# Kernel tuning notes

Hardware: AMD Instinct MI355X
Metric: run time of the kernel (lower is better)

## Reference

```python
import jax, jax.numpy as jnp
import numpy as np

EPS = 1e-5  # torch BatchNorm2d default eps
K = 3       # kernel_size
D = 1       # dilation (== padding)


def setup_inputs() -> dict:
    key = jax.random.key(0)
    k0, k1, k2 = jax.random.split(key, 3)
    N, C, H, W, O = 4, 2048, 32, 32, 256
    return {
        "x": jax.random.normal(k0, (N, C, H, W), jnp.float32),
        "conv_w": jax.random.normal(k1, (K * K, C, K, K), jnp.float32) * 0.01,
        "gamma": jnp.ones((K * K,), jnp.float32),
        "beta": jnp.zeros((K * K,), jnp.float32),
        "weight": jax.random.normal(k2, (O, C, K * K), jnp.float32) * 0.01,
    }


def reference(x, conv_w, gamma, beta, weight):
    n, c, h, w = x.shape
    # --- dynamic-kernel generator: conv (stride 1, pad=dilation) -> BN (train mode) -> softmax over K*K ---
    sigma = jax.lax.conv_general_dilated(
        x, conv_w, window_strides=(1, 1), padding=[(D, D), (D, D)],
        rhs_dilation=(D, D), dimension_numbers=("NCHW", "OIHW", "NCHW"))  # (n, K*K, h, w)
    mean = sigma.mean(axis=(0, 2, 3), keepdims=True)
    var = sigma.var(axis=(0, 2, 3), keepdims=True)  # biased variance, as torch BN uses for normalization
    sigma = (sigma - mean) * jax.lax.rsqrt(var + EPS)
    sigma = sigma * gamma[None, :, None, None] + beta[None, :, None, None]
    sigma = jax.nn.softmax(sigma, axis=1)            # softmax over the K*K kernel positions
    sigma = sigma.reshape(n, K * K, h * w)           # (n, K*K, h*w)
    # --- unfold (im2col), channel-major (C, kh, kw) ordering matching torch F.unfold ---
    patches = jax.lax.conv_general_dilated_patches(
        x, (K, K), (1, 1), [(D, D), (D, D)], rhs_dilation=(D, D),
        dimension_numbers=("NCHW", "OIHW", "NCHW"))  # (n, C*K*K, h, w)
    patches = patches.reshape(n, c, K * K, h * w)     # (n, C, K*K, h*w)
    # --- per-pixel dynamic weighting + learned projection ---
    # out[n,o,m] = sum_{c,l} patches[n,c,l,m] * sigma[n,l,m] * weight[o,c,l]
    out = jnp.einsum("nclm,nlm,ocl->nom", patches, sigma, weight)
    return out.reshape(n, weight.shape[0], h, w)
```

## Files before the change

kernel.cpp:

```cpp
#include <hip/hip_runtime.h>
#include <hip/hip_bf16.h>
#include <stdint.h>

typedef unsigned short u16;
typedef __attribute__((ext_vector_type(8))) short short8;
typedef __attribute__((ext_vector_type(4))) float floatx4;

#define N_IMG 4
#define C_IN  2048
#define HW    1024
#define KK    9
#define O_OUT 256
#define NPIX  4096
#define M_PAD  2432
#define K_DIM  2048
#define BN_EPS 1e-5f

#define OFF_A    0u
#define OFF_XT   9961472u
#define OFF_H    26738688u
#define OFF_SRAW 46661632u
#define OFF_STAT 46809088u

__device__ __forceinline__ u16 f2b(float f) {
    unsigned u = __float_as_uint(f);
    return (u16)((u + 0x7FFFu + ((u >> 16) & 1u)) >> 16);
}

__device__ __forceinline__ void load8f(const float* base, size_t eidx, u16* out) {
    const float* p = base + eidx;
    float4 a = ((const float4*)p)[0];
    float4 b = ((const float4*)p)[1];
    float f[8] = {a.x, a.y, a.z, a.w, b.x, b.y, b.z, b.w};
#pragma unroll
    for (int j = 0; j < 8; ++j) out[j] = f2b(f[j]);
}

__global__ void build_all(const float* __restrict__ x, const float* __restrict__ wgt,
                          const float* __restrict__ cw, u16* __restrict__ xt,
                          u16* __restrict__ A, float* __restrict__ stats) {
    __shared__ __align__(16) u16 lds[9 * 2056];
    int b = blockIdx.x, t = threadIdx.x;
    if (b < 2048) {
        int c0 = (b & 31) * 64, p0 = ((b >> 5) & 15) * 64, n = b >> 9;
        int r = t >> 3, pv = (t & 7) * 8;
        u16 h0[8], h1[8];
        load8f(x, (size_t)(n * C_IN + c0 + r) * HW + p0 + pv, h0);
        load8f(x, (size_t)(n * C_IN + c0 + r + 32) * HW + p0 + pv, h1);
#pragma unroll
        for (int j = 0; j < 8; ++j) {
            lds[(pv + j) * 72 + r]      = h0[j];
            lds[(pv + j) * 72 + r + 32] = h1[j];
        }
        __syncthreads();
        int pr = t >> 3, cv = (t & 7) * 8;
        uint4 o0 = *(const uint4*)&lds[pr * 72 + cv];
        uint4 o1 = *(const uint4*)&lds[(pr + 32) * 72 + cv];
        *(uint4*)(xt + (size_t)(n * HW + p0 + pr) * K_DIM + c0 + cv) = o0;
        *(uint4*)(xt + (size_t)(n * HW + p0 + pr + 32) * K_DIM + c0 + cv) = o1;
    } else if (b < 2304) {
        int o = b - 2048;
        size_t base = (size_t)o * 18432;
        for (int i = 0; i < 9; ++i) {
            int e0 = (t + i * 256) * 8;
            u16 hv[8];
            load8f(wgt, base + e0, hv);
#pragma unroll
            for (int j = 0; j < 8; ++j) {
                int e = e0 + j;
                int c = e / 9, l = e - c * 9;
                lds[l * 2056 + c] = hv[j];
            }
        }
        __syncthreads();
        for (int l = 0; l < 9; ++l) {
            size_t row = (size_t)l * 256 + o;
            *(uint4*)(A + row * K_DIM + t * 8) = *(const uint4*)&lds[l * 2056 + t * 8];
        }
    } else if (b < 2313) {
        int l = b - 2304;
        size_t base = (size_t)l * 18432;
        for (int i = 0; i < 9; ++i) {
            int e0 = (t + i * 256) * 8;
            u16 hv[8];
            load8f(cw, base + e0, hv);
#pragma unroll
            for (int j = 0; j < 8; ++j) {
                int e = e0 + j;
                int c = e / 9, k = e - c * 9;
                lds[k * 2056 + c] = hv[j];
            }
        }
        __syncthreads();
        for (int k = 0; k < 9; ++k) {
            size_t row = 2304 + (size_t)k * 9 + l;
            *(uint4*)(A + row * K_DIM + t * 8) = *(const uint4*)&lds[k * 2056 + t * 8];
        }
    } else {
        uint4 z = {0, 0, 0, 0};
        uint4* dst = (uint4*)(A + (size_t)2385 * K_DIM);
        for (int i = t; i < (47 * 2048) / 8; i += 256) dst[i] = z;
        if (t < 18) stats[t] = 0.0f;
    }
}

__device__ __forceinline__ void gload_lds16(const void* g, void* l) {
    __builtin_amdgcn_global_load_lds((__attribute__((address_space(1))) void*)(g),
                                     (__attribute__((address_space(3))) void*)(l), 16, 0, 0);
}

__global__ void gemm_bt(const u16* __restrict__ A, const u16* __restrict__ B,
                        __hip_bfloat16* __restrict__ C) {
    __shared__ __align__(16) u16 As[128 * 32];
    __shared__ __align__(16) u16 Bs[128 * 32];
    int bx = blockIdx.x;
    int mt = bx % 19, nt = bx / 19;
    int m0 = mt * 128, n0 = nt * 128;
    int t = threadIdx.x;
    int w = t >> 6, lam = t & 63;
    int wm = w >> 1, wn = w & 1;
    int lm = lam & 15, q = lam >> 4;

    floatx4 acc[4][4];
    floatx4 z = {0.f, 0.f, 0.f, 0.f};
#pragma unroll
    for (int i = 0; i < 4; ++i)
#pragma unroll
        for (int j = 0; j < 4; ++j) acc[i][j] = z;

    int c0 = w, c1 = w + 4;
    int rrow0 = c0 * 16 + (lam >> 2);
    int rrow1 = c1 * 16 + (lam >> 2);
    int kc = (lam & 3) * 8;
    const u16* gA0 = A + (size_t)(m0 + rrow0) * K_DIM + kc;
    const u16* gA1 = A + (size_t)(m0 + rrow1) * K_DIM + kc;
    const u16* gB0 = B + (size_t)(n0 + rrow0) * K_DIM + kc;
    const u16* gB1 = B + (size_t)(n0 + rrow1) * K_DIM + kc;
    u16* lA0 = As + c0 * 512;  u16* lA1 = As + c1 * 512;
    u16* lB0 = Bs + c0 * 512;  u16* lB1 = Bs + c1 * 512;

    for (int kt = 0; kt < K_DIM / 32; ++kt) {
        gload_lds16(gA0, lA0);
        gload_lds16(gA1, lA1);
        gload_lds16(gB0, lB0);
        gload_lds16(gB1, lB1);
        gA0 += 32; gA1 += 32; gB0 += 32; gB1 += 32;
        __syncthreads();
        short8 af[4], bf[4];
#pragma unroll
        for (int i = 0; i < 4; ++i)
            af[i] = *(const short8*)(As + (wm * 64 + i * 16 + lm) * 32 + q * 8);
#pragma unroll
        for (int j = 0; j < 4; ++j)
            bf[j] = *(const short8*)(Bs + (wn * 64 + j * 16 + lm) * 32 + q * 8);
#pragma unroll
        for (int i = 0; i < 4; ++i)
#pragma unroll
            for (int j = 0; j < 4; ++j)
                acc[i][j] = __builtin_amdgcn_mfma_f32_16x16x32_bf16(af[i], bf[j], acc[i][j], 0, 0, 0);
        __syncthreads();
    }
#pragma unroll
    for (int i = 0; i < 4; ++i) {
        int gm = m0 + wm * 64 + i * 16 + q * 4;
#pragma unroll
        for (int j = 0; j < 4; ++j) {
            int gn = n0 + wn * 64 + j * 16 + lm;
#pragma unroll
            for (int r = 0; r < 4; ++r)
                C[(size_t)(gm + r) * NPIX + gn] = __float2bfloat16(acc[i][j][r]);
        }
    }
}

__global__ void sigma_stats(const __hip_bfloat16* __restrict__ Hm, float* __restrict__ sraw,
                            float* __restrict__ stats) {
    int b = blockIdx.x;
    int qq = b & 3, nl = b >> 2;
    int n = nl / 9, l = nl - n * 9;
    int t = threadIdx.x;
    int pix = qq * 256 + t;
    int y = pix >> 5, x = pix & 31;
    float v = 0.f;
#pragma unroll
    for (int k = 0; k < 9; ++k) {
        int yy = y + k / 3 - 1, xx = x + (k % 3) - 1;
        if (yy >= 0 && yy < 32 && xx >= 0 && xx < 32)
            v += __bfloat162float(Hm[(size_t)(2304 + k * 9 + l) * NPIX + n * HW + yy * 32 + xx]);
    }
    sraw[(size_t)nl * HW + pix] = v;
    __shared__ float r1[256], r2[256];
    r1[t] = v; r2[t] = v * v;
    __syncthreads();
    for (int s = 128; s > 0; s >>= 1) {
        if (t < s) { r1[t] += r1[t + s]; r2[t] += r2[t + s]; }
        __syncthreads();
    }
    if (t == 0) { atomicAdd(&stats[l], r1[0]); atomicAdd(&stats[9 + l], r2[0]); }
}

__global__ void tail(const __hip_bfloat16* __restrict__ Hm, const float* __restrict__ sraw,
                     const float* __restrict__ stats, const float* __restrict__ gamma,
                     const float* __restrict__ beta, float* __restrict__ out) {
    int b = blockIdx.x;
    int n = b >> 8, o = b & 255;
    int t = threadIdx.x;
    float mean[9], istd[9], gg[9], bb[9];
#pragma unroll
    for (int l = 0; l < 9; ++l) {
        float m = stats[l] * (1.f / 4096.f);
        float var = stats[9 + l] * (1.f / 4096.f) - m * m;
        mean[l] = m; istd[l] = rsqrtf(var + BN_EPS);
        gg[l] = gamma[l]; bb[l] = beta[l];
    }
    for (int i = 0; i < 4; ++i) {
        int pix = t + i * 256;
        int y = pix >> 5, x = pix & 31;
        float v[9];
        float mx = -1e30f;
#pragma unroll
        for (int l = 0; l < 9; ++l) {
            float tv = (sraw[(size_t)(n * 9 + l) * HW + pix] - mean[l]) * istd[l];
            tv = tv * gg[l] + bb[l];
            v[l] = tv; mx = fmaxf(mx, tv);
        }
        float ssum = 0.f;
#pragma unroll
        for (int l = 0; l < 9; ++l) { v[l] = __expf(v[l] - mx); ssum += v[l]; }
        float inv = 1.f / ssum;
        float acc = 0.f;
#pragma unroll
        for (int l = 0; l < 9; ++l) {
            int dy = l / 3 - 1, dx = l % 3 - 1;
            int yy = y + dy, xx = x + dx;
            if (yy >= 0 && yy < 32 && xx >= 0 && xx < 32) {
                float h = __bfloat162float(Hm[(size_t)(l * 256 + o) * NPIX + n * HW + yy * 32 + xx]);
                acc += v[l] * inv * h;
            }
        }
        out[((size_t)n * 256 + o) * HW + pix] = acc;
    }
}

extern "C" void kernel_launch(void* const* d_in, const int* in_sizes, int n_in,
                              void* d_out, int out_size, void* d_ws, size_t ws_size,
                              hipStream_t stream) {
    const float* x     = (const float*)d_in[0];
    const float* cw    = (const float*)d_in[1];
    const float* gamma = (const float*)d_in[2];
    const float* beta  = (const float*)d_in[3];
    const float* wgt   = (const float*)d_in[4];

    char* ws = (char*)d_ws;
    u16*   Abuf = (u16*)(ws + OFF_A);
    u16*   XT   = (u16*)(ws + OFF_XT);
    u16*   Hm   = (u16*)(ws + OFF_H);
    float* sraw = (float*)(ws + OFF_SRAW);
    float* stats= (float*)(ws + OFF_STAT);

    build_all<<<2314, 256, 0, stream>>>(x, wgt, cw, XT, Abuf, stats);
    gemm_bt<<<19 * 32, 256, 0, stream>>>(Abuf, XT, (__hip_bfloat16*)Hm);
    sigma_stats<<<N_IMG * KK * 4, 256, 0, stream>>>((const __hip_bfloat16*)Hm, sraw, stats);
    tail<<<N_IMG * O_OUT, 256, 0, stream>>>((const __hip_bfloat16*)Hm, sraw, stats, gamma, beta, (float*)d_out);
}
```

Measured before the change: 176.7 us.

## Split GEMM K dimension in two, pack transpose LDS, process two outputs per tail thread

When the workspace is large enough, the GEMM is split along K into two halves. Each half writes its own bf16 partial output, which doubles the block count (608 to 1216) and fills more CUs. The downstream sigma_stats and tail kernels sum the two partials when reading. The build transpose now packs two channels per 32-bit LDS word with a padded stride, and the tail kernel computes two output channels per block and hoists the softmax weights and offsets. The cost is extra H traffic from the second partial buffer, plus a small loss of precision from rounding each half to bf16.

```diff
diff --git a/kernel.cpp b/kernel.cpp
--- a/kernel.cpp
+++ b/kernel.cpp
@@ -16,11 +16,10 @@
 #define K_DIM  2048
 #define BN_EPS 1e-5f
 
-#define OFF_A    0u
-#define OFF_XT   9961472u
-#define OFF_H    26738688u
-#define OFF_SRAW 46661632u
-#define OFF_STAT 46809088u
+#define SZ_A   ((size_t)M_PAD * K_DIM * 2)
+#define SZ_XT  ((size_t)NPIX * K_DIM * 2)
+#define SZ_H   ((size_t)M_PAD * NPIX * 2)
+#define SZ_SRAW ((size_t)N_IMG * KK * HW * 4)
 
 __device__ __forceinline__ u16 f2b(float f) {
     unsigned u = __float_as_uint(f);
@@ -43,21 +42,25 @@
     int b = blockIdx.x, t = threadIdx.x;
     if (b < 2048) {
         int c0 = (b & 31) * 64, p0 = ((b >> 5) & 15) * 64, n = b >> 9;
-        int r = t >> 3, pv = (t & 7) * 8;
+        int rp = t >> 3;
+        int pv = (t & 7) * 8;
         u16 h0[8], h1[8];
-        load8f(x, (size_t)(n * C_IN + c0 + r) * HW + p0 + pv, h0);
-        load8f(x, (size_t)(n * C_IN + c0 + r + 32) * HW + p0 + pv, h1);
-#pragma unroll
-        for (int j = 0; j < 8; ++j) {
-            lds[(pv + j) * 72 + r]      = h0[j];
-            lds[(pv + j) * 72 + r + 32] = h1[j];
-        }
-        __syncthreads();
-        int pr = t >> 3, cv = (t & 7) * 8;
-        uint4 o0 = *(const uint4*)&lds[pr * 72 + cv];
-        uint4 o1 = *(const uint4*)&lds[(pr + 32) * 72 + cv];
-        *(uint4*)(xt + (size_t)(n * HW + p0 + pr) * K_DIM + c0 + cv) = o0;
-        *(uint4*)(xt + (size_t)(n * HW + p0 + pr + 32) * K_DIM + c0 + cv) = o1;
+        load8f(x, (size_t)(n * C_IN + c0 + 2 * rp) * HW + p0 + pv, h0);
+        load8f(x, (size_t)(n * C_IN + c0 + 2 * rp + 1) * HW + p0 + pv, h1);
+        unsigned* l32 = (unsigned*)lds;
+#pragma unroll
+        for (int j = 0; j < 8; ++j)
+            l32[(pv + j) * 35 + rp] = (unsigned)h0[j] | ((unsigned)h1[j] << 16);
+        __syncthreads();
+        int pr = t >> 3, cq = (t & 7) * 4;
+        unsigned o0[4], o1[4];
+#pragma unroll
+        for (int i = 0; i < 4; ++i) {
+            o0[i] = l32[pr * 35 + cq + i];
+            o1[i] = l32[(pr + 32) * 35 + cq + i];
+        }
+        *(uint4*)(xt + (size_t)(n * HW + p0 + pr) * K_DIM + c0 + cq * 2) = *(uint4*)o0;
+        *(uint4*)(xt + (size_t)(n * HW + p0 + pr + 32) * K_DIM + c0 + cq * 2) = *(uint4*)o1;
     } else if (b < 2304) {
         int o = b - 2048;
         size_t base = (size_t)o * 18432;
@@ -110,11 +113,20 @@
 }
 
 __global__ void gemm_bt(const u16* __restrict__ A, const u16* __restrict__ B,
-                        __hip_bfloat16* __restrict__ C) {
+                        __hip_bfloat16* __restrict__ C, int split) {
     __shared__ __align__(16) u16 As[128 * 32];
     __shared__ __align__(16) u16 Bs[128 * 32];
     int bx = blockIdx.x;
-    int mt = bx % 19, nt = bx / 19;
+    int tile, kbase, iters;
+    __hip_bfloat16* Cw;
+    if (split) {
+        int ks = bx & 1; tile = bx >> 1;
+        kbase = ks * (K_DIM / 2); iters = K_DIM / 64;
+        Cw = C + (size_t)ks * M_PAD * NPIX;
+    } else {
+        tile = bx; kbase = 0; iters = K_DIM / 32; Cw = C;
+    }
+    int mt = tile % 19, nt = tile / 19;
     int m0 = mt * 128, n0 = nt * 128;
     int t = threadIdx.x;
     int w = t >> 6, lam = t & 63;
@@ -132,14 +144,14 @@
     int rrow0 = c0 * 16 + (lam >> 2);
     int rrow1 = c1 * 16 + (lam >> 2);
     int kc = (lam & 3) * 8;
-    const u16* gA0 = A + (size_t)(m0 + rrow0) * K_DIM + kc;
-    const u16* gA1 = A + (size_t)(m0 + rrow1) * K_DIM + kc;
-    const u16* gB0 = B + (size_t)(n0 + rrow0) * K_DIM + kc;
-    const u16* gB1 = B + (size_t)(n0 + rrow1) * K_DIM + kc;
+    const u16* gA0 = A + (size_t)(m0 + rrow0) * K_DIM + kbase + kc;
+    const u16* gA1 = A + (size_t)(m0 + rrow1) * K_DIM + kbase + kc;
+    const u16* gB0 = B + (size_t)(n0 + rrow0) * K_DIM + kbase + kc;
+    const u16* gB1 = B + (size_t)(n0 + rrow1) * K_DIM + kbase + kc;
     u16* lA0 = As + c0 * 512;  u16* lA1 = As + c1 * 512;
     u16* lB0 = Bs + c0 * 512;  u16* lB1 = Bs + c1 * 512;
 
-    for (int kt = 0; kt < K_DIM / 32; ++kt) {
+    for (int kt = 0; kt < iters; ++kt) {
         gload_lds16(gA0, lA0);
         gload_lds16(gA1, lA1);
         gload_lds16(gB0, lB0);
@@ -168,13 +180,13 @@
             int gn = n0 + wn * 64 + j * 16 + lm;
 #pragma unroll
             for (int r = 0; r < 4; ++r)
-                C[(size_t)(gm + r) * NPIX + gn] = __float2bfloat16(acc[i][j][r]);
-        }
-    }
-}
-
-__global__ void sigma_stats(const __hip_bfloat16* __restrict__ Hm, float* __restrict__ sraw,
-                            float* __restrict__ stats) {
+                Cw[(size_t)(gm + r) * NPIX + gn] = __float2bfloat16(acc[i][j][r]);
+        }
+    }
+}
+
+__global__ void sigma_stats(const __hip_bfloat16* __restrict__ H0, const __hip_bfloat16* __restrict__ H1,
+                            float* __restrict__ sraw, float* __restrict__ stats, int split) {
     int b = blockIdx.x;
     int qq = b & 3, nl = b >> 2;
     int n = nl / 9, l = nl - n * 9;
@@ -185,8 +197,12 @@
 #pragma unroll
     for (int k = 0; k < 9; ++k) {
         int yy = y + k / 3 - 1, xx = x + (k % 3) - 1;
-        if (yy >= 0 && yy < 32 && xx >= 0 && xx < 32)
-            v += __bfloat162float(Hm[(size_t)(2304 + k * 9 + l) * NPIX + n * HW + yy * 32 + xx]);
+        if (yy >= 0 && yy < 32 && xx >= 0 && xx < 32) {
+            size_t idx = (size_t)(2304 + k * 9 + l) * NPIX + n * HW + yy * 32 + xx;
+            float h = __bfloat162float(H0[idx]);
+            if (split) h += __bfloat162float(H1[idx]);
+            v += h;
+        }
     }
     sraw[(size_t)nl * HW + pix] = v;
     __shared__ float r1[256], r2[256];
@@ -199,11 +215,12 @@
     if (t == 0) { atomicAdd(&stats[l], r1[0]); atomicAdd(&stats[9 + l], r2[0]); }
 }
 
-__global__ void tail(const __hip_bfloat16* __restrict__ Hm, const float* __restrict__ sraw,
-                     const float* __restrict__ stats, const float* __restrict__ gamma,
-                     const float* __restrict__ beta, float* __restrict__ out) {
+__global__ void tail(const __hip_bfloat16* __restrict__ H0, const __hip_bfloat16* __restrict__ H1,
+                     const float* __restrict__ sraw, const float* __restrict__ stats,
+                     const float* __restrict__ gamma, const float* __restrict__ beta,
+                     float* __restrict__ out, int split) {
     int b = blockIdx.x;
-    int n = b >> 8, o = b & 255;
+    int n = b >> 7, og = b & 127;
     int t = threadIdx.x;
     float mean[9], istd[9], gg[9], bb[9];
 #pragma unroll
@@ -228,17 +245,28 @@
 #pragma unroll
         for (int l = 0; l < 9; ++l) { v[l] = __expf(v[l] - mx); ssum += v[l]; }
         float inv = 1.f / ssum;
-        float acc = 0.f;
+        float sv[9]; int sp[9];
 #pragma unroll
         for (int l = 0; l < 9; ++l) {
             int dy = l / 3 - 1, dx = l % 3 - 1;
             int yy = y + dy, xx = x + dx;
-            if (yy >= 0 && yy < 32 && xx >= 0 && xx < 32) {
-                float h = __bfloat162float(Hm[(size_t)(l * 256 + o) * NPIX + n * HW + yy * 32 + xx]);
-                acc += v[l] * inv * h;
+            bool ok = (yy >= 0 && yy < 32 && xx >= 0 && xx < 32);
+            sp[l] = ok ? (pix + dy * 32 + dx) : pix;
+            sv[l] = ok ? v[l] * inv : 0.f;
+        }
+#pragma unroll
+        for (int oj = 0; oj < 2; ++oj) {
+            int o = og * 2 + oj;
+            float acc = 0.f;
+#pragma unroll
+            for (int l = 0; l < 9; ++l) {
+                size_t idx = (size_t)(l * 256 + o) * NPIX + n * HW + sp[l];
+                float h = __bfloat162float(H0[idx]);
+                if (split) h += __bfloat162float(H1[idx]);
+                acc += sv[l] * h;
             }
-        }
-        out[((size_t)n * 256 + o) * HW + pix] = acc;
+            out[((size_t)n * 256 + o) * HW + pix] = acc;
+        }
     }
 }
 
@@ -252,14 +280,21 @@
     const float* wgt   = (const float*)d_in[4];
 
     char* ws = (char*)d_ws;
-    u16*   Abuf = (u16*)(ws + OFF_A);
-    u16*   XT   = (u16*)(ws + OFF_XT);
-    u16*   Hm   = (u16*)(ws + OFF_H);
-    float* sraw = (float*)(ws + OFF_SRAW);
-    float* stats= (float*)(ws + OFF_STAT);
+    u16* Abuf = (u16*)(ws);
+    u16* XT   = (u16*)(ws + SZ_A);
+    u16* H0   = (u16*)(ws + SZ_A + SZ_XT);
+
+    size_t need_split = SZ_A + SZ_XT + 2 * SZ_H + SZ_SRAW + 256;
+    int split = (ws_size >= need_split) ? 1 : 0;
+    u16*   H1    = split ? (u16*)(ws + SZ_A + SZ_XT + SZ_H) : H0;
+    char*  rest  = ws + SZ_A + SZ_XT + (split ? 2 : 1) * SZ_H;
+    float* sraw  = (float*)rest;
+    float* stats = (float*)(rest + SZ_SRAW);
 
     build_all<<<2314, 256, 0, stream>>>(x, wgt, cw, XT, Abuf, stats);
-    gemm_bt<<<19 * 32, 256, 0, stream>>>(Abuf, XT, (__hip_bfloat16*)Hm);
-    sigma_stats<<<N_IMG * KK * 4, 256, 0, stream>>>((const __hip_bfloat16*)Hm, sraw, stats);
-    tail<<<N_IMG * O_OUT, 256, 0, stream>>>((const __hip_bfloat16*)Hm, sraw, stats, gamma, beta, (float*)d_out);
-}
+    gemm_bt<<<split ? 1216 : 608, 256, 0, stream>>>(Abuf, XT, (__hip_bfloat16*)H0, split);
+    sigma_stats<<<N_IMG * KK * 4, 256, 0, stream>>>((const __hip_bfloat16*)H0, (const __hip_bfloat16*)H1,
+                                                    sraw, stats, split);
+    tail<<<N_IMG * 128, 256, 0, stream>>>((const __hip_bfloat16*)H0, (const __hip_bfloat16*)H1,
+                                          sraw, stats, gamma, beta, (float*)d_out, split);
+}
```

Result: slower. 209.9 us (+18.8%).
